# Optimization experiments

Hardware: AMD Instinct MI355X
Metric: run time of the kernel (lower is better)

## Reference

```python
import math
import jax, jax.numpy as jnp
import numpy as np

SCALE = 64.0
MARGIN = 0.5
T = 0.2
COS_M = math.cos(MARGIN)
SIN_M = math.sin(MARGIN)
TH = math.cos(math.pi - MARGIN)
MM = math.sin(math.pi - MARGIN) * MARGIN
EPS = 1e-07

B, D, C = 512, 512, 100000


def setup_inputs() -> dict:
    key = jax.random.key(0)
    k1, k2, k3 = jax.random.split(key, 3)
    embedding = jax.random.normal(k1, (B, D), dtype=jnp.float32)
    # xavier_uniform for (num_classes, embed_size)
    limit = math.sqrt(6.0 / (C + D))
    weight = jax.random.uniform(k2, (C, D), dtype=jnp.float32, minval=-limit, maxval=limit)
    ground_truth = jax.random.randint(k3, (B,), 0, C, dtype=jnp.int64)
    return {"embedding": embedding, "weight": weight, "ground_truth": ground_truth}


def reference(embedding, weight, ground_truth):
    gt = ground_truth.astype(jnp.int32)
    e = embedding / jnp.linalg.norm(embedding, axis=1, keepdims=True)
    w = weight / jnp.linalg.norm(weight, axis=1, keepdims=True)
    # (B, C) cosine similarities
    cos_theta = jnp.clip(jnp.einsum('bd,cd->bc', e, w), -1.0 + EPS, 1.0 - EPS)
    pos = jnp.take_along_axis(cos_theta, gt[:, None], axis=1)  # (B, 1)
    sin_theta = jnp.sqrt(jnp.clip(1.0 - pos * pos, EPS, 1.0 - EPS))
    phi = pos * COS_M - sin_theta * SIN_M
    phi = jnp.where(pos > TH, phi, pos - MM)  # easy_margin=False branch
    # hard-example reweighting: fixed=False -> (t+1)*cos + t where cos > phi
    mask = cos_theta > phi  # phi broadcasts (B,1) -> (B,C)
    cos_theta = jnp.where(mask, (T + 1.0) * cos_theta + T, cos_theta)
    # scatter phi into the ground-truth column
    output = cos_theta.at[jnp.arange(B), gt].set(phi[:, 0])
    output = output * SCALE
    # mean cross-entropy
    logp = jax.nn.log_softmax(output, axis=1)
    loss = -jnp.mean(jnp.take_along_axis(logp, gt[:, None], axis=1))
    return loss
```

## Files before the change

kernel.cpp:

```cpp
#include <hip/hip_runtime.h>
#include <hip/hip_bf16.h>
#include <stdint.h>

typedef unsigned short u16;
typedef __attribute__((ext_vector_type(8))) short short8;
typedef __attribute__((ext_vector_type(4))) float floatx4;

#define B_   512
#define D_   512
#define C_   100000

#define SCALE_  64.0f
#define COSM_   0.8775825618903728f
#define SINM_   0.479425538604203f
#define TH_     (-0.8775825618903728f)
#define MM_     0.2397127693021015f
#define EPS_    1e-7f
#define SHIFT_  89.6f

#define BN 64
#define BK 32

__device__ inline float wave_reduce_sum(float v) {
    v += __shfl_xor(v, 1);
    v += __shfl_xor(v, 2);
    v += __shfl_xor(v, 4);
    v += __shfl_xor(v, 8);
    v += __shfl_xor(v, 16);
    v += __shfl_xor(v, 32);
    return v;
}

__device__ inline u16 f2bf(float x) {
    union { float f; uint32_t u; } v; v.f = x;
    uint32_t r = v.u + 0x7fffu + ((v.u >> 16) & 1u);
    return (u16)(r >> 16);
}

__global__ __launch_bounds__(256) void norm_e_phi_kernel(
    const float* __restrict__ emb, const float* __restrict__ w_raw,
    const int* __restrict__ gt, u16* __restrict__ e_bf16,
    float* __restrict__ phi) {
    int wv = threadIdx.x >> 6;
    int lane = threadIdx.x & 63;
    int b = blockIdx.x * 4 + wv;
    const float4* rp = (const float4*)(emb + (long)b * D_);
    float4 f0 = rp[lane], f1 = rp[lane + 64];
    float sq = f0.x*f0.x + f0.y*f0.y + f0.z*f0.z + f0.w*f0.w
             + f1.x*f1.x + f1.y*f1.y + f1.z*f1.z + f1.w*f1.w;
    sq = wave_reduce_sum(sq);
    float rn = 1.0f / sqrtf(sq);
    f0.x *= rn; f0.y *= rn; f0.z *= rn; f0.w *= rn;
    f1.x *= rn; f1.y *= rn; f1.z *= rn; f1.w *= rn;
    uint2 p0, p1;
    p0.x = (uint32_t)f2bf(f0.x) | ((uint32_t)f2bf(f0.y) << 16);
    p0.y = (uint32_t)f2bf(f0.z) | ((uint32_t)f2bf(f0.w) << 16);
    p1.x = (uint32_t)f2bf(f1.x) | ((uint32_t)f2bf(f1.y) << 16);
    p1.y = (uint32_t)f2bf(f1.z) | ((uint32_t)f2bf(f1.w) << 16);
    uint2* ob = (uint2*)(e_bf16 + (long)b * D_);
    ob[lane] = p0;
    ob[lane + 64] = p1;

    int g = gt[b];
    const float4* wp = (const float4*)(w_raw + (long)g * D_);
    float4 w0 = wp[lane], w1 = wp[lane + 64];
    float dt = f0.x*w0.x + f0.y*w0.y + f0.z*w0.z + f0.w*w0.w
             + f1.x*w1.x + f1.y*w1.y + f1.z*w1.z + f1.w*w1.w;
    float wsq = w0.x*w0.x + w0.y*w0.y + w0.z*w0.z + w0.w*w0.w
              + w1.x*w1.x + w1.y*w1.y + w1.z*w1.z + w1.w*w1.w;
    dt = wave_reduce_sum(dt);
    wsq = wave_reduce_sum(wsq);
    if (lane == 0) {
        float pos = dt / sqrtf(wsq);
        pos = fminf(fmaxf(pos, -1.0f + EPS_), 1.0f - EPS_);
        float s2 = 1.0f - pos * pos;
        s2 = fminf(fmaxf(s2, EPS_), 1.0f - EPS_);
        float sin_t = sqrtf(s2);
        float ph = pos * COSM_ - sin_t * SINM_;
        ph = (pos > TH_) ? ph : (pos - MM_);
        phi[b] = ph;
    }
}

__global__ __launch_bounds__(256, 2) void gemm_arcface_fused(
    const u16* __restrict__ a_g,
    const float* __restrict__ w_g,
    const float* __restrict__ phi, const int* __restrict__ gt,
    float* __restrict__ rowsum) {
    __shared__ __align__(16) u16 b_tile[2][BN * BK];
    __shared__ float phi_s[B_];
    __shared__ int gt_s[B_];
    __shared__ float rnorm_s[BN];

    int tid = threadIdx.x;
    int c0 = blockIdx.x * BN;
    phi_s[tid] = phi[tid];
    phi_s[tid + 256] = phi[tid + 256];
    gt_s[tid] = gt[tid];
    gt_s[tid + 256] = gt[tid + 256];

    int rb = tid >> 2;
    int bslot = tid & 3;
    int bkq = bslot ^ ((tid >> 3) & 3);
    long brow_g = min(c0 + rb, C_ - 1);
    const float4* b_src = (const float4*)(w_g + brow_g * (long)D_ + bkq * 8);

    int wv = tid >> 6, lane = tid & 63;
    int low4 = lane & 15, quad = lane >> 4;
    int wm = wv * 128;
    int lslot = quad ^ ((low4 >> 1) & 3);

    const u16* a_base = a_g + (long)(wm + low4) * D_ + quad * 8;
    int bf_off = low4 * BK + lslot * 8;

    floatx4 acc[8][4] = {};
    float sq = 0.0f;

    float4 bv0 = b_src[0], bv1 = b_src[1];
    short8 afc[8];
#pragma unroll
    for (int mi = 0; mi < 8; mi++)
        afc[mi] = *(const short8*)(a_base + mi * 16 * D_);
    {
        union { u16 h[8]; uint4 q; } u;
        u.h[0] = f2bf(bv0.x); u.h[1] = f2bf(bv0.y);
        u.h[2] = f2bf(bv0.z); u.h[3] = f2bf(bv0.w);
        u.h[4] = f2bf(bv1.x); u.h[5] = f2bf(bv1.y);
        u.h[6] = f2bf(bv1.z); u.h[7] = f2bf(bv1.w);
        *(uint4*)&b_tile[0][rb * BK + bslot * 8] = u.q;
        sq += bv0.x*bv0.x + bv0.y*bv0.y + bv0.z*bv0.z + bv0.w*bv0.w
            + bv1.x*bv1.x + bv1.y*bv1.y + bv1.z*bv1.z + bv1.w*bv1.w;
    }
    __syncthreads();

#pragma unroll
    for (int kt = 0; kt < 16; kt++) {
        int p = kt & 1;
        short8 afn[8];
        float4 nv0, nv1;
        if (kt < 15) {
            nv0 = b_src[(kt + 1) * 8];
            nv1 = b_src[(kt + 1) * 8 + 1];
#pragma unroll
            for (int mi = 0; mi < 8; mi++)
                afn[mi] = *(const short8*)(a_base + mi * 16 * D_ + (kt + 1) * BK);
        }
        short8 bf[4];
#pragma unroll
        for (int ni = 0; ni < 4; ni++)
            bf[ni] = *(const short8*)(&b_tile[p][ni * 16 * BK + bf_off]);
#pragma unroll
        for (int mi = 0; mi < 8; mi++)
#pragma unroll
            for (int ni = 0; ni < 4; ni++)
                acc[mi][ni] = __builtin_amdgcn_mfma_f32_16x16x32_bf16(
                    afc[mi], bf[ni], acc[mi][ni], 0, 0, 0);
        if (kt < 15) {
            union { u16 h[8]; uint4 q; } u;
            u.h[0] = f2bf(nv0.x); u.h[1] = f2bf(nv0.y);
            u.h[2] = f2bf(nv0.z); u.h[3] = f2bf(nv0.w);
            u.h[4] = f2bf(nv1.x); u.h[5] = f2bf(nv1.y);
            u.h[6] = f2bf(nv1.z); u.h[7] = f2bf(nv1.w);
            *(uint4*)&b_tile[1 - p][rb * BK + bslot * 8] = u.q;
            sq += nv0.x*nv0.x + nv0.y*nv0.y + nv0.z*nv0.z + nv0.w*nv0.w
                + nv1.x*nv1.x + nv1.y*nv1.y + nv1.z*nv1.z + nv1.w*nv1.w;
#pragma unroll
            for (int mi = 0; mi < 8; mi++) afc[mi] = afn[mi];
        }
        __syncthreads();
    }

    sq += __shfl_xor(sq, 1);
    sq += __shfl_xor(sq, 2);
    if ((tid & 3) == 0) rnorm_s[rb] = 1.0f / sqrtf(sq);
    __syncthreads();

#pragma unroll
    for (int mi = 0; mi < 8; mi++) {
#pragma unroll
        for (int r = 0; r < 4; r++) {
            int row = wm + mi * 16 + quad * 4 + r;
            float ph = phi_s[row];
            int g = gt_s[row];
            float s = 0.0f;
#pragma unroll
            for (int ni = 0; ni < 4; ni++) {
                int cl = ni * 16 + low4;
                int c = c0 + cl;
                float v = acc[mi][ni][r] * rnorm_s[cl];
                v = fminf(fmaxf(v, -1.0f + EPS_), 1.0f - EPS_);
                float logit = (v > ph) ? (1.2f * v + 0.2f) : v;
                logit *= SCALE_;
                if (c == g) logit = SCALE_ * ph;
                s += (c < C_) ? __expf(logit - SHIFT_) : 0.0f;
            }
            s += __shfl_xor(s, 1);
            s += __shfl_xor(s, 2);
            s += __shfl_xor(s, 4);
            s += __shfl_xor(s, 8);
            if (low4 == 0) atomicAdd(&rowsum[row], s);
        }
    }
}

__global__ __launch_bounds__(256) void loss_kernel(
    const float* __restrict__ rowsum, const float* __restrict__ phi,
    float* __restrict__ out) {
    __shared__ float red[4];
    int tid = threadIdx.x;
    float s = 0.0f;
    for (int b = tid; b < B_; b += 256)
        s += logf(rowsum[b]) + SHIFT_ - SCALE_ * phi[b];
    s = wave_reduce_sum(s);
    int wv = tid >> 6, lane = tid & 63;
    if (lane == 0) red[wv] = s;
    __syncthreads();
    if (tid == 0) out[0] = (red[0] + red[1] + red[2] + red[3]) * (1.0f / B_);
}

extern "C" void kernel_launch(void* const* d_in, const int* in_sizes, int n_in,
                              void* d_out, int out_size, void* d_ws, size_t ws_size,
                              hipStream_t stream) {
    const float* emb = (const float*)d_in[0];
    const float* wgt = (const float*)d_in[1];
    const int* gt = (const int*)d_in[2];
    float* out = (float*)d_out;

    char* ws = (char*)d_ws;
    u16* e_bf16 = (u16*)(ws);
    float* phi = (float*)(ws + 524288);
    float* rowsum = (float*)(ws + 526336);

    norm_e_phi_kernel<<<B_ / 4, 256, 0, stream>>>(emb, wgt, gt, e_bf16, phi);
    hipMemsetAsync(rowsum, 0, B_ * sizeof(float), stream);
    gemm_arcface_fused<<<(C_ + BN - 1) / BN, 256, 0, stream>>>(
        e_bf16, wgt, phi, gt, rowsum);
    loss_kernel<<<1, 256, 0, stream>>>(rowsum, phi, out);
}
```

Baseline: 463.2 us.

## Split batch dimension across two blocks, deepen W prefetch, fold rowsum zeroing

Each GEMM block now covers half the batch rows (256) instead of all 512, which halves the accumulator registers and doubles the grid. Launch bounds move to 3 blocks per SM for more occupancy. The W prefetch is deepened to two tiles ahead, and A fragments are loaded directly each iteration instead of through a register double buffer. The rowsum memset is folded into the normalization kernel. The trade-off is that every W tile is now loaded and converted to bf16 twice (once per batch half), which doubles fp32 weight traffic unless L2 absorbs the repeat.

```diff
diff --git a/kernel.cpp b/kernel.cpp
--- a/kernel.cpp
+++ b/kernel.cpp
@@ -18,6 +18,7 @@
 #define EPS_    1e-7f
 #define SHIFT_  89.6f
 
+#define BM 256
 #define BN 64
 #define BK 32
 
@@ -40,7 +41,8 @@
 __global__ __launch_bounds__(256) void norm_e_phi_kernel(
     const float* __restrict__ emb, const float* __restrict__ w_raw,
     const int* __restrict__ gt, u16* __restrict__ e_bf16,
-    float* __restrict__ phi) {
+    float* __restrict__ phi, float* __restrict__ rowsum) {
+    if (threadIdx.x < 4) rowsum[blockIdx.x * 4 + threadIdx.x] = 0.0f;
     int wv = threadIdx.x >> 6;
     int lane = threadIdx.x & 63;
     int b = blockIdx.x * 4 + wv;
@@ -82,91 +84,81 @@
     }
 }
 
-__global__ __launch_bounds__(256, 2) void gemm_arcface_fused(
+__device__ inline void cvt_store(const float4& v0, const float4& v1,
+                                 u16* dst, float& sq) {
+    union { u16 h[8]; uint4 q; } u;
+    u.h[0] = f2bf(v0.x); u.h[1] = f2bf(v0.y);
+    u.h[2] = f2bf(v0.z); u.h[3] = f2bf(v0.w);
+    u.h[4] = f2bf(v1.x); u.h[5] = f2bf(v1.y);
+    u.h[6] = f2bf(v1.z); u.h[7] = f2bf(v1.w);
+    *(uint4*)dst = u.q;
+    sq += v0.x*v0.x + v0.y*v0.y + v0.z*v0.z + v0.w*v0.w
+        + v1.x*v1.x + v1.y*v1.y + v1.z*v1.z + v1.w*v1.w;
+}
+
+__global__ __launch_bounds__(256, 3) void gemm_arcface_fused(
     const u16* __restrict__ a_g,
     const float* __restrict__ w_g,
     const float* __restrict__ phi, const int* __restrict__ gt,
     float* __restrict__ rowsum) {
     __shared__ __align__(16) u16 b_tile[2][BN * BK];
-    __shared__ float phi_s[B_];
-    __shared__ int gt_s[B_];
+    __shared__ float phi_s[BM];
+    __shared__ int gt_s[BM];
     __shared__ float rnorm_s[BN];
 
     int tid = threadIdx.x;
-    int c0 = blockIdx.x * BN;
-    phi_s[tid] = phi[tid];
-    phi_s[tid + 256] = phi[tid + 256];
-    gt_s[tid] = gt[tid];
-    gt_s[tid + 256] = gt[tid + 256];
+    int c0 = (blockIdx.x >> 1) * BN;
+    int m0 = (blockIdx.x & 1) * BM;
+
+    phi_s[tid] = phi[m0 + tid];
+    gt_s[tid] = gt[m0 + tid];
 
     int rb = tid >> 2;
     int bslot = tid & 3;
-    int bkq = bslot ^ ((tid >> 3) & 3);
+    int bkq = bslot ^ ((rb >> 1) & 3);
     long brow_g = min(c0 + rb, C_ - 1);
     const float4* b_src = (const float4*)(w_g + brow_g * (long)D_ + bkq * 8);
+    u16* b_dst0 = &b_tile[0][rb * BK + bslot * 8];
+    u16* b_dst1 = &b_tile[1][rb * BK + bslot * 8];
 
     int wv = tid >> 6, lane = tid & 63;
     int low4 = lane & 15, quad = lane >> 4;
-    int wm = wv * 128;
     int lslot = quad ^ ((low4 >> 1) & 3);
-
-    const u16* a_base = a_g + (long)(wm + low4) * D_ + quad * 8;
+    const u16* a_base = a_g + (long)(m0 + wv * 64 + low4) * D_ + quad * 8;
     int bf_off = low4 * BK + lslot * 8;
 
-    floatx4 acc[8][4] = {};
+    floatx4 acc[4][4] = {};
     float sq = 0.0f;
-
-    float4 bv0 = b_src[0], bv1 = b_src[1];
-    short8 afc[8];
-#pragma unroll
-    for (int mi = 0; mi < 8; mi++)
-        afc[mi] = *(const short8*)(a_base + mi * 16 * D_);
-    {
-        union { u16 h[8]; uint4 q; } u;
-        u.h[0] = f2bf(bv0.x); u.h[1] = f2bf(bv0.y);
-        u.h[2] = f2bf(bv0.z); u.h[3] = f2bf(bv0.w);
-        u.h[4] = f2bf(bv1.x); u.h[5] = f2bf(bv1.y);
-        u.h[6] = f2bf(bv1.z); u.h[7] = f2bf(bv1.w);
-        *(uint4*)&b_tile[0][rb * BK + bslot * 8] = u.q;
-        sq += bv0.x*bv0.x + bv0.y*bv0.y + bv0.z*bv0.z + bv0.w*bv0.w
-            + bv1.x*bv1.x + bv1.y*bv1.y + bv1.z*bv1.z + bv1.w*bv1.w;
-    }
+    float4 bv[2][2];
+    short8 afc[4];
+
+    bv[0][0] = b_src[0]; bv[0][1] = b_src[1];
+    cvt_store(bv[0][0], bv[0][1], b_dst0, sq);
+    bv[1][0] = b_src[8]; bv[1][1] = b_src[9];
     __syncthreads();
 
 #pragma unroll
     for (int kt = 0; kt < 16; kt++) {
         int p = kt & 1;
-        short8 afn[8];
-        float4 nv0, nv1;
-        if (kt < 15) {
-            nv0 = b_src[(kt + 1) * 8];
-            nv1 = b_src[(kt + 1) * 8 + 1];
-#pragma unroll
-            for (int mi = 0; mi < 8; mi++)
-                afn[mi] = *(const short8*)(a_base + mi * 16 * D_ + (kt + 1) * BK);
+        if (kt < 14) {
+            bv[p][0] = b_src[(kt + 2) * 8];
+            bv[p][1] = b_src[(kt + 2) * 8 + 1];
         }
+#pragma unroll
+        for (int mi = 0; mi < 4; mi++)
+            afc[mi] = *(const short8*)(a_base + (long)mi * 16 * D_ + kt * BK);
         short8 bf[4];
 #pragma unroll
         for (int ni = 0; ni < 4; ni++)
             bf[ni] = *(const short8*)(&b_tile[p][ni * 16 * BK + bf_off]);
 #pragma unroll
-        for (int mi = 0; mi < 8; mi++)
+        for (int mi = 0; mi < 4; mi++)
 #pragma unroll
             for (int ni = 0; ni < 4; ni++)
                 acc[mi][ni] = __builtin_amdgcn_mfma_f32_16x16x32_bf16(
                     afc[mi], bf[ni], acc[mi][ni], 0, 0, 0);
-        if (kt < 15) {
-            union { u16 h[8]; uint4 q; } u;
-            u.h[0] = f2bf(nv0.x); u.h[1] = f2bf(nv0.y);
-            u.h[2] = f2bf(nv0.z); u.h[3] = f2bf(nv0.w);
-            u.h[4] = f2bf(nv1.x); u.h[5] = f2bf(nv1.y);
-            u.h[6] = f2bf(nv1.z); u.h[7] = f2bf(nv1.w);
-            *(uint4*)&b_tile[1 - p][rb * BK + bslot * 8] = u.q;
-            sq += nv0.x*nv0.x + nv0.y*nv0.y + nv0.z*nv0.z + nv0.w*nv0.w
-                + nv1.x*nv1.x + nv1.y*nv1.y + nv1.z*nv1.z + nv1.w*nv1.w;
-#pragma unroll
-            for (int mi = 0; mi < 8; mi++) afc[mi] = afn[mi];
-        }
+        if (kt < 15)
+            cvt_store(bv[1 - p][0], bv[1 - p][1], p ? b_dst0 : b_dst1, sq);
         __syncthreads();
     }
 
@@ -176,12 +168,12 @@
     __syncthreads();
 
 #pragma unroll
-    for (int mi = 0; mi < 8; mi++) {
+    for (int mi = 0; mi < 4; mi++) {
 #pragma unroll
         for (int r = 0; r < 4; r++) {
-            int row = wm + mi * 16 + quad * 4 + r;
-            float ph = phi_s[row];
-            int g = gt_s[row];
+            int rl = wv * 64 + mi * 16 + quad * 4 + r;
+            float ph = phi_s[rl];
+            int g = gt_s[rl];
             float s = 0.0f;
 #pragma unroll
             for (int ni = 0; ni < 4; ni++) {
@@ -198,7 +190,7 @@
             s += __shfl_xor(s, 2);
             s += __shfl_xor(s, 4);
             s += __shfl_xor(s, 8);
-            if (low4 == 0) atomicAdd(&rowsum[row], s);
+            if (low4 == 0) atomicAdd(&rowsum[m0 + rl], s);
         }
     }
 }
@@ -231,9 +223,8 @@
     float* phi = (float*)(ws + 524288);
     float* rowsum = (float*)(ws + 526336);
 
-    norm_e_phi_kernel<<<B_ / 4, 256, 0, stream>>>(emb, wgt, gt, e_bf16, phi);
-    hipMemsetAsync(rowsum, 0, B_ * sizeof(float), stream);
-    gemm_arcface_fused<<<(C_ + BN - 1) / BN, 256, 0, stream>>>(
-        e_bf16, wgt, phi, gt, rowsum);
+    norm_e_phi_kernel<<<B_ / 4, 256, 0, stream>>>(emb, wgt, gt, e_bf16, phi, rowsum);
+    int nc = (C_ + BN - 1) / BN;
+    gemm_arcface_fused<<<nc * 2, 256, 0, stream>>>(e_bf16, wgt, phi, gt, rowsum);
     loss_kernel<<<1, 256, 0, stream>>>(rowsum, phi, out);
 }
```

New measurement: 449.1 us. -3.1%, faster.
